# Kernel tuning notes

Measured on AMD Instinct MI355X. Metric: run time of the kernel, lower is better.

Reference implementation:

```python
import jax, jax.numpy as jnp
import numpy as np

B, S, H = 8, 512, 1024          # batch, seq_len, hidden_size
T, K, FF = 8, 2, 4096           # num_thoughts, top_k, ffn dim (4*H)
NH = 8                          # combiner attention heads
HD = H // NH
CREATIVITY = 1.0


def setup_inputs() -> dict:
    key = jax.random.key(0)
    ks = jax.random.split(key, 16)
    s = 0.02
    return {
        "hidden_states": jax.random.normal(ks[0], (B, S, H), jnp.float32),
        # router
        "router_w": jax.random.normal(ks[1], (H, T), jnp.float32) * s,
        "router_b": jnp.zeros((T,), jnp.float32),
        # thought branch FFNs (one per thought)
        "W1": jax.random.normal(ks[2], (T, H, FF), jnp.float32) * s,
        "b1": jnp.zeros((T, FF), jnp.float32),
        "W2": jax.random.normal(ks[3], (T, FF, H), jnp.float32) * s,
        "b2": jnp.zeros((T, H), jnp.float32),
        # attention combiner (MultiheadAttention proj weights)
        "Wq": jax.random.normal(ks[4], (H, H), jnp.float32) * s,
        "bq": jnp.zeros((H,), jnp.float32),
        "Wk": jax.random.normal(ks[5], (H, H), jnp.float32) * s,
        "bk": jnp.zeros((H,), jnp.float32),
        "Wv": jax.random.normal(ks[6], (H, H), jnp.float32) * s,
        "bv": jnp.zeros((H,), jnp.float32),
        "Wo": jax.random.normal(ks[7], (H, H), jnp.float32) * s,
        "bo": jnp.zeros((H,), jnp.float32),
    }


def reference(hidden_states, router_w, router_b, W1, b1, W2, b2,
              Wq, bq, Wk, bk, Wv, bv, Wo, bo):
    # ---- router: mean-pool -> linear -> softmax -> top-k ----
    pooled = hidden_states.mean(axis=1)                       # [B,H]
    router_probs = jax.nn.softmax(pooled @ router_w + router_b, axis=-1)  # [B,T]
    top_p, top_i = jax.lax.top_k(router_probs, K)             # [B,K]
    weights = jax.nn.softmax(top_p, axis=-1)                  # renormalized active weights [B,K]

    # ---- grouped branch FFN (gather expert weights, batched GEMMs) ----
    h = jnp.einsum('bsh,bkhf->bksf', hidden_states, W1[top_i]) + b1[top_i][:, :, None, :]
    h = jax.nn.gelu(h, approximate=False)
    branch_out = jnp.einsum('bksf,bkfh->bksh', h, W2[top_i]) + b2[top_i][:, :, None, :]
    branch_out = branch_out * CREATIVITY                      # [B,K,S,H]

    # ---- attention combiner over flattened thoughts [B, K*S, H] ----
    L = K * S
    flat = branch_out.reshape(B, L, H)
    q = (flat @ Wq + bq).reshape(B, L, NH, HD)
    k = (flat @ Wk + bk).reshape(B, L, NH, HD)
    v = (flat @ Wv + bv).reshape(B, L, NH, HD)
    scores = jnp.einsum('blhd,bmhd->bhlm', q, k) / jnp.sqrt(jnp.float32(HD))
    attn = jax.nn.softmax(scores, axis=-1)
    ctx = jnp.einsum('bhlm,bmhd->blhd', attn, v).reshape(B, L, H)
    attended = (ctx @ Wo + bo).reshape(B, K, S, H)

    combined = jnp.einsum('bksh,bk->bsh', attended, weights)  # [B,S,H]

    # ---- metrics ----
    entropy = jnp.mean(-jnp.sum(router_probs * jnp.log(router_probs + 1e-8), axis=1))
    a = branch_out[:, 0].reshape(B, -1)
    b_ = branch_out[:, 1].reshape(B, -1)
    cos = jnp.sum(a * b_, -1) / jnp.maximum(
        jnp.linalg.norm(a, axis=-1) * jnp.linalg.norm(b_, axis=-1), 1e-8)
    diversity = jnp.mean(1.0 - cos)
    return combined, entropy, diversity
```

## Files before the change

### kernel.cpp

```cpp
#include <hip/hip_runtime.h>
#include <hip/hip_bf16.h>
#include <math.h>

typedef float f32x4 __attribute__((ext_vector_type(4)));
typedef short s16x8 __attribute__((ext_vector_type(8)));
typedef short s16x4 __attribute__((ext_vector_type(4)));
typedef unsigned int u32;

#define DEVI __device__ __forceinline__

#define Bn   8
#define Sn   512
#define Hn   1024
#define Tn   8
#define Kn   2
#define FFn  4096
#define NHn  8
#define HDn  128
#define Ln   1024
#define OUT_COMBINED 4194304

DEVI unsigned short f2bf(float x) {
  __hip_bfloat16 h = __float2bfloat16(x);
  union { __hip_bfloat16 h; unsigned short u; } cv; cv.h = h; return cv.u;
}
DEVI float bf2f(unsigned short u) {
  union { u32 i; float f; } cv; cv.i = ((u32)u) << 16; return cv.f;
}

typedef __attribute__((address_space(3))) u32 lds_u32;
typedef __attribute__((address_space(1))) u32 glb_u32;
DEVI void gload16(const void* g, void* l) {
  __builtin_amdgcn_global_load_lds((const glb_u32*)g, (lds_u32*)l, 16, 0, 0);
}

__global__ __launch_bounds__(256) void pool_part_k(const float* __restrict__ hid, float* __restrict__ part)
{
  const int b = blockIdx.x, scn = blockIdx.y;
  const int hh = threadIdx.x * 4;
  float4 acc = make_float4(0.f, 0.f, 0.f, 0.f);
  const float* base = hid + ((long)b * Sn + (long)scn * 128) * Hn + hh;
  for (int s = 0; s < 128; ++s) {
    float4 v = *(const float4*)(base + (long)s * Hn);
    acc.x += v.x; acc.y += v.y; acc.z += v.z; acc.w += v.w;
  }
  *(float4*)(part + ((long)(scn * Bn + b)) * Hn + hh) = acc;
}

__global__ __launch_bounds__(256) void pool_final_k(const float* __restrict__ part, float* __restrict__ pooled)
{
  const int i = blockIdx.x * 256 + threadIdx.x;
  float s = 0.f;
  for (int sc = 0; sc < 4; ++sc) s += part[sc * (Bn * Hn) + i];
  pooled[i] = s * (1.f / (float)Sn);
}

__global__ __launch_bounds__(256) void router_k(
    const float* __restrict__ pooled, const float* __restrict__ rw, const float* __restrict__ rb,
    float* __restrict__ probs, int* __restrict__ topi, float* __restrict__ wts,
    int* __restrict__ flags, float* __restrict__ entropy_out)
{
  __shared__ float partial[256];
  __shared__ float lg[64];
  __shared__ int sfl[8];
  __shared__ float sent[8];
  const int tid = threadIdx.x;
  const int bt = tid & 63, slice = tid >> 6;
  const int b = bt >> 3, t = bt & 7;
  if (tid < 8) sfl[tid] = 0;
  float acc = 0.f;
  const float* pb = pooled + b * Hn;
  for (int i = slice * 256; i < slice * 256 + 256; ++i) acc += pb[i] * rw[i * Tn + t];
  partial[tid] = acc;
  __syncthreads();
  if (tid < 64) lg[tid] = rb[t] + partial[tid] + partial[tid + 64] + partial[tid + 128] + partial[tid + 192];
  __syncthreads();
  if (tid < 64 && t == 0) {
    float p[8];
    float mx = lg[b * 8];
    for (int i = 1; i < 8; ++i) mx = fmaxf(mx, lg[b * 8 + i]);
    float ssum = 0.f;
    for (int i = 0; i < 8; ++i) { p[i] = expf(lg[b * 8 + i] - mx); ssum += p[i]; }
    float ent = 0.f;
    for (int i = 0; i < 8; ++i) { p[i] /= ssum; ent -= p[i] * logf(p[i] + 1e-8f); probs[b * 8 + i] = p[i]; }
    sent[b] = ent;
    int i1 = 0;
    for (int i = 1; i < 8; ++i) if (p[i] > p[i1]) i1 = i;
    int i2 = (i1 == 0) ? 1 : 0;
    for (int i = 0; i < 8; ++i) if (i != i1 && p[i] > p[i2]) i2 = i;
    float w0 = 1.f / (1.f + expf(p[i2] - p[i1]));
    float w1 = 1.f / (1.f + expf(p[i1] - p[i2]));
    topi[b * 2] = i1; topi[b * 2 + 1] = i2;
    wts[b * 2] = w0; wts[b * 2 + 1] = w1;
    atomicOr(&sfl[i1], 1); atomicOr(&sfl[i2], 1);
  }
  __syncthreads();
  if (tid < 8) flags[tid] = sfl[tid];
  if (tid == 0) {
    float e = 0.f;
    for (int i = 0; i < 8; ++i) e += sent[i];
    entropy_out[0] = e * (1.f / (float)Bn);
  }
}

__global__ __launch_bounds__(256) void cvt_k(const float* __restrict__ in, unsigned short* __restrict__ out)
{
  const long i = ((long)blockIdx.x * 256 + threadIdx.x) * 4;
  float4 v = *(const float4*)(in + i);
  s16x4 o;
  o[0] = (short)f2bf(v.x); o[1] = (short)f2bf(v.y); o[2] = (short)f2bf(v.z); o[3] = (short)f2bf(v.w);
  *(s16x4*)(out + i) = o;
}

__global__ __launch_bounds__(256) void bias3_k(const float* __restrict__ bq, const float* __restrict__ bk,
                                               const float* __restrict__ bv, float* __restrict__ o)
{
  const int i = blockIdx.x * 256 + threadIdx.x;
  o[i] = bq[i]; o[i + 1024] = bk[i]; o[i + 2048] = bv[i];
}

__global__ __launch_bounds__(256) void transpose_k(const float* __restrict__ Win, unsigned short* __restrict__ Wout,
                                                   int Kd, int N, long sIn, long sOut, const int* __restrict__ flags)
{
  const int t = blockIdx.z;
  if (flags && flags[t] == 0) return;
  __shared__ float tile[64][65];
  const float* in = Win + (long)t * sIn;
  unsigned short* out = Wout + (long)t * sOut;
  const int kb = blockIdx.y * 64, nb = blockIdx.x * 64;
  const int tx = threadIdx.x & 15, ty = threadIdx.x >> 4;
  #pragma unroll
  for (int i = 0; i < 4; ++i) {
    const int r = ty + i * 16;
    float4 v = *(const float4*)(in + (long)(kb + r) * N + nb + tx * 4);
    tile[r][tx * 4 + 0] = v.x; tile[r][tx * 4 + 1] = v.y;
    tile[r][tx * 4 + 2] = v.z; tile[r][tx * 4 + 3] = v.w;
  }
  __syncthreads();
  #pragma unroll
  for (int i = 0; i < 4; ++i) {
    const int n = ty + i * 16;
    s16x4 o;
    #pragma unroll
    for (int j = 0; j < 4; ++j) o[j] = (short)f2bf(tile[tx * 4 + j][n]);
    *(s16x4*)(out + (long)(nb + n) * Kd + kb + tx * 4) = o;
  }
}

template<int WM, int EPI, int OUTMODE>
__global__ __launch_bounds__(WM * 256, 2) void gemm256_k(
    const unsigned short* __restrict__ A0, const unsigned short* __restrict__ Bt0,
    const float* __restrict__ bias0, unsigned short* __restrict__ C0,
    int N, int Kd,
    const int* __restrict__ topi, int kTop,
    long sA_b, long sA_p, long sBt_t, int sBias_t, long sC_p)
{
  constexpr int NBUF = (WM == 2) ? 4 : 3;
  constexpr int ASZ = WM * 8192;
  constexpr int BSZ = 16384;
  constexpr int BISS = 4 / WM;
  __shared__ __align__(16) char smem[NBUF * (ASZ + BSZ)];
  char* const Ab = smem;
  char* const Bb = smem + NBUF * ASZ;

  const int z = blockIdx.z;
  const int bidx = kTop ? (z / kTop) : 0;
  const int te = topi ? topi[z] : 0;
  const unsigned short* A = A0 + (long)bidx * sA_b + (long)z * sA_p;
  const unsigned short* Bt = Bt0 + (long)te * sBt_t;
  const float* bias = bias0 + (long)te * sBias_t;
  unsigned short* C = C0 + (long)z * sC_p;

  const int m0 = blockIdx.y * (WM * 128);
  const int n0 = blockIdx.x * 256;
  const int tid = threadIdx.x;
  const int lane = tid & 63, w = tid >> 6;
  const int wm = w >> 2, wn = w & 3;
  const int rA = lane & 15, g = lane >> 4;

  const int srow = tid >> 2;
  const int sc   = tid & 3;
  const unsigned short* gA[2];
  #pragma unroll
  for (int i = 0; i < 2; ++i) {
    const int r = i * (WM * 64) + srow;
    gA[i] = A + (long)(m0 + r) * Kd + ((sc ^ ((r >> 1) & 3)) * 8);
  }
  const unsigned short* gB[BISS];
  #pragma unroll
  for (int i = 0; i < BISS; ++i) {
    const int r = i * (WM * 64) + srow;
    gB[i] = Bt + (long)(n0 + r) * Kd + ((sc ^ ((r >> 1) & 3)) * 8);
  }
  const int sdo = tid * 16;

  int aoff[8], boff[4];
  #pragma unroll
  for (int mi = 0; mi < 8; ++mi) {
    const int row = wm * 128 + mi * 16 + rA;
    aoff[mi] = row * 64 + ((g ^ ((row >> 1) & 3)) << 4);
  }
  #pragma unroll
  for (int nj = 0; nj < 4; ++nj) {
    const int row = wn * 64 + nj * 16 + rA;
    boff[nj] = row * 64 + ((g ^ ((row >> 1) & 3)) << 4);
  }

  f32x4 acc[8][4];
  const f32x4 zero = {0.f, 0.f, 0.f, 0.f};
  #pragma unroll
  for (int i = 0; i < 8; ++i)
    #pragma unroll
    for (int j = 0; j < 4; ++j) acc[i][j] = zero;

  const int nt = Kd >> 5;

  for (int j = 0; j < NBUF - 1; ++j) {
    #pragma unroll
    for (int i = 0; i < 2; ++i)
      gload16(gA[i] + j * 32, Ab + j * ASZ + i * (WM * 4096) + sdo);
    #pragma unroll
    for (int i = 0; i < BISS; ++i)
      gload16(gB[i] + j * 32, Bb + j * BSZ + i * (WM * 4096) + sdo);
  }
  if constexpr (WM == 2) asm volatile("s_waitcnt vmcnt(8)" ::: "memory");
  else                   asm volatile("s_waitcnt vmcnt(6)" ::: "memory");
  __builtin_amdgcn_s_barrier();

  int cb = 0;
  for (int kt = 0; kt < nt; ++kt) {
    const char* pa = Ab + cb * ASZ;
    const char* pb = Bb + cb * BSZ;
    const int ft = kt + NBUF - 1;
    const int fb = (cb == 0) ? NBUF - 1 : cb - 1;
    const bool st = (ft < nt);

    s16x8 af[4], bf[4];
    #pragma unroll
    for (int mi = 0; mi < 4; ++mi) af[mi] = *(const s16x8*)(pa + aoff[mi]);
    #pragma unroll
    for (int nj = 0; nj < 4; ++nj) bf[nj] = *(const s16x8*)(pb + boff[nj]);
    if (st) {
      #pragma unroll
      for (int i = 0; i < 2; ++i)
        gload16(gA[i] + ft * 32, Ab + fb * ASZ + i * (WM * 4096) + sdo);
      if constexpr (WM == 1)
        gload16(gB[0] + ft * 32, Bb + fb * BSZ + sdo);
    }
    asm volatile("" ::: "memory");
    __builtin_amdgcn_s_barrier();
    __builtin_amdgcn_s_setprio(1);
    #pragma unroll
    for (int mi = 0; mi < 4; ++mi)
      #pragma unroll
      for (int nj = 0; nj < 4; ++nj)
        acc[mi][nj] = __builtin_amdgcn_mfma_f32_16x16x32_bf16(af[mi], bf[nj], acc[mi][nj], 0, 0, 0);
    __builtin_amdgcn_s_setprio(0);
    __builtin_amdgcn_s_barrier();

    s16x8 af2[4];
    #pragma unroll
    for (int mi = 0; mi < 4; ++mi) af2[mi] = *(const s16x8*)(pa + aoff[4 + mi]);
    if (st) {
      if constexpr (WM == 2) {
        gload16(gB[0] + ft * 32, Bb + fb * BSZ + sdo);
        gload16(gB[1] + ft * 32, Bb + fb * BSZ + 8192 + sdo);
      } else {
        gload16(gB[1] + ft * 32, Bb + fb * BSZ + 4096 + sdo);
        gload16(gB[2] + ft * 32, Bb + fb * BSZ + 8192 + sdo);
        gload16(gB[3] + ft * 32, Bb + fb * BSZ + 12288 + sdo);
      }
    }
    asm volatile("" ::: "memory");
    __builtin_amdgcn_s_barrier();
    __builtin_amdgcn_s_setprio(1);
    #pragma unroll
    for (int mi = 0; mi < 4; ++mi)
      #pragma unroll
      for (int nj = 0; nj < 4; ++nj)
        acc[4 + mi][nj] = __builtin_amdgcn_mfma_f32_16x16x32_bf16(af2[mi], bf[nj], acc[4 + mi][nj], 0, 0, 0);
    __builtin_amdgcn_s_setprio(0);

    if constexpr (WM == 2) {
      if (kt < nt - 3)       asm volatile("s_waitcnt vmcnt(8)" ::: "memory");
      else if (kt == nt - 3) asm volatile("s_waitcnt vmcnt(4)" ::: "memory");
      else if (kt == nt - 2) asm volatile("s_waitcnt vmcnt(0)" ::: "memory");
    } else {
      if (kt < nt - 2)       asm volatile("s_waitcnt vmcnt(6)" ::: "memory");
      else if (kt == nt - 2) asm volatile("s_waitcnt vmcnt(0)" ::: "memory");
    }
    __builtin_amdgcn_s_barrier();
    cb = (cb + 1 == NBUF) ? 0 : cb + 1;
  }

  __syncthreads();

  unsigned short* et = (unsigned short*)(smem + w * 9216);
  const int r4 = (lane >> 4) << 2;
  const int nbase = n0 + wn * 64;
  const int seg = (OUTMODE == 1) ? (nbase >> 10) : 0;
  const int erow = lane >> 3, echunk = lane & 7;
  float bv[4];
  #pragma unroll
  for (int nj = 0; nj < 4; ++nj) bv[nj] = bias[nbase + nj * 16 + rA];

  #pragma unroll
  for (int p = 0; p < 2; ++p) {
    #pragma unroll
    for (int nj = 0; nj < 4; ++nj) {
      #pragma unroll
      for (int mi2 = 0; mi2 < 4; ++mi2) {
        #pragma unroll
        for (int j = 0; j < 4; ++j) {
          float x = acc[p * 4 + mi2][nj][j] + bv[nj];
          if (EPI == 1) x = 0.5f * x * (1.0f + erff(x * 0.70710678118654752f));
          const int mrl = mi2 * 16 + r4 + j;
          const int ncl = nj * 16 + rA;
          if (OUTMODE == 0 || seg < 2) et[mrl * 72 + ncl] = f2bf(x);
          else                         et[ncl * 72 + mrl] = f2bf(x);
        }
      }
    }
    const long mrow0 = m0 + wm * 128 + p * 64;
    if (OUTMODE == 0) {
      #pragma unroll
      for (int rr = 0; rr < 8; ++rr) {
        const int row = rr * 8 + erow;
        s16x8 v = *(const s16x8*)(et + row * 72 + echunk * 8);
        *(s16x8*)(C + (mrow0 + row) * N + nbase + echunk * 8) = v;
      }
    } else {
      const int nseg = nbase & 1023;
      if (seg < 2) {
        unsigned short* dst = C + (long)seg * 8388608;
        #pragma unroll
        for (int rr = 0; rr < 8; ++rr) {
          const int row = rr * 8 + erow;
          s16x8 v = *(const s16x8*)(et + row * 72 + echunk * 8);
          *(s16x8*)(dst + (mrow0 + row) * 1024 + nseg + echunk * 8) = v;
        }
      } else {
        unsigned short* vtp = C + 16777216;
        const int bb = (int)(mrow0 >> 10);
        const int ltok0 = (int)(mrow0 & 1023);
        #pragma unroll
        for (int rr = 0; rr < 8; ++rr) {
          const int nrow = rr * 8 + erow;
          s16x8 v = *(const s16x8*)(et + nrow * 72 + echunk * 8);
          *(s16x8*)(vtp + ((long)(bb * 1024 + nseg + nrow)) * 1024 + ltok0 + echunk * 8) = v;
        }
      }
    }
  }
}

__global__ __launch_bounds__(256) void flash_k(
    const unsigned short* __restrict__ q, const unsigned short* __restrict__ k,
    const unsigned short* __restrict__ vt, unsigned short* __restrict__ ctx)
{
  __shared__ unsigned short Ks[64 * 128];
  __shared__ unsigned short Vs[128 * 64];
  __shared__ unsigned short Ps[4][32 * 72];
  const int qt = blockIdx.x, h = blockIdx.y, b = blockIdx.z;
  const int tid = threadIdx.x, lane = tid & 63, w = tid >> 6;
  const int rA = lane & 15, g = lane >> 4;
  const int q0w = qt * 128 + w * 32;

  s16x8 qf[2][4];
  #pragma unroll
  for (int qi = 0; qi < 2; ++qi) {
    const unsigned short* qp = q + ((long)(b * Ln + q0w + qi * 16 + rA)) * Hn + h * HDn + g * 8;
    #pragma unroll
    for (int kk = 0; kk < 4; ++kk) qf[qi][kk] = *(const s16x8*)(qp + kk * 32);
  }

  f32x4 o[2][8];
  const f32x4 zero = {0.f, 0.f, 0.f, 0.f};
  #pragma unroll
  for (int qi = 0; qi < 2; ++qi)
    #pragma unroll
    for (int nn = 0; nn < 8; ++nn) o[qi][nn] = zero;
  float lrun[2][4];
  #pragma unroll
  for (int qi = 0; qi < 2; ++qi)
    #pragma unroll
    for (int j = 0; j < 4; ++j) lrun[qi][j] = 0.f;
  float m = 0.f;

  const float sc2 = 0.08838834764831845f * 1.4426950408889634f;

  const int krow0 = w * 16 + g;
  const int kc = lane & 15;
  const int vrow0 = w * 32 + (lane >> 3);
  const int vc = lane & 7;

  for (int kvt = 0; kvt < 16; ++kvt) {
    const int kv0 = kvt * 64;
    __syncthreads();
    #pragma unroll
    for (int qq = 0; qq < 4; ++qq) {
      const int rk = krow0 + qq * 4;
      gload16(k + ((long)(b * Ln + kv0 + rk)) * Hn + h * HDn + ((kc ^ (rk & 7)) * 8),
              (char*)Ks + w * 4096 + qq * 1024);
      const int rv = vrow0 + qq * 8;
      gload16(vt + ((long)(b * 1024 + h * HDn + rv)) * Ln + kv0 + ((vc ^ (rv & 7)) * 8),
              (char*)Vs + w * 4096 + qq * 1024);
    }
    __syncthreads();

    f32x4 sacc[2][4];
    #pragma unroll
    for (int qi = 0; qi < 2; ++qi)
      #pragma unroll
      for (int nj = 0; nj < 4; ++nj) sacc[qi][nj] = zero;
    #pragma unroll
    for (int kk = 0; kk < 4; ++kk) {
      #pragma unroll
      for (int nj = 0; nj < 4; ++nj) {
        const int row = nj * 16 + rA;
        const int byt = row * 256 + (((kk * 4 + g) ^ (row & 7)) << 4);
        s16x8 kf = *(const s16x8*)((const char*)Ks + byt);
        sacc[0][nj] = __builtin_amdgcn_mfma_f32_16x16x32_bf16(qf[0][kk], kf, sacc[0][nj], 0, 0, 0);
        sacc[1][nj] = __builtin_amdgcn_mfma_f32_16x16x32_bf16(qf[1][kk], kf, sacc[1][nj], 0, 0, 0);
      }
    }

    float vmax = -3.0e38f;
    #pragma unroll
    for (int qi = 0; qi < 2; ++qi)
      #pragma unroll
      for (int nj = 0; nj < 4; ++nj)
        #pragma unroll
        for (int j = 0; j < 4; ++j) {
          const float s = sacc[qi][nj][j] * sc2;
          sacc[qi][nj][j] = s;
          vmax = fmaxf(vmax, s);
        }
    if (!__all(vmax <= m + 8.0f)) {
      float mn = vmax;
      #pragma unroll
      for (int mm = 1; mm < 64; mm <<= 1) mn = fmaxf(mn, __shfl_xor(mn, mm, 64));
      const float al = exp2f(m - mn);
      #pragma unroll
      for (int qi = 0; qi < 2; ++qi) {
        #pragma unroll
        for (int nn = 0; nn < 8; ++nn)
          #pragma unroll
          for (int j = 0; j < 4; ++j) o[qi][nn][j] *= al;
        #pragma unroll
        for (int j = 0; j < 4; ++j) lrun[qi][j] *= al;
      }
      m = mn;
    }
    #pragma unroll
    for (int qi = 0; qi < 2; ++qi)
      #pragma unroll
      for (int j = 0; j < 4; ++j) {
        float p0 = exp2f(sacc[qi][0][j] - m);
        float p1 = exp2f(sacc[qi][1][j] - m);
        float p2 = exp2f(sacc[qi][2][j] - m);
        float p3 = exp2f(sacc[qi][3][j] - m);
        lrun[qi][j] += (p0 + p1) + (p2 + p3);
        const int prow = (qi * 16 + g * 4 + j) * 72;
        Ps[w][prow + 0 * 16 + rA] = f2bf(p0);
        Ps[w][prow + 1 * 16 + rA] = f2bf(p1);
        Ps[w][prow + 2 * 16 + rA] = f2bf(p2);
        Ps[w][prow + 3 * 16 + rA] = f2bf(p3);
      }

    s16x8 pf[2][2];
    #pragma unroll
    for (int qi = 0; qi < 2; ++qi)
      #pragma unroll
      for (int kk2 = 0; kk2 < 2; ++kk2)
        pf[qi][kk2] = *(const s16x8*)(&Ps[w][(qi * 16 + rA) * 72 + kk2 * 32 + g * 8]);
    #pragma unroll
    for (int kk2 = 0; kk2 < 2; ++kk2) {
      #pragma unroll
      for (int nn = 0; nn < 8; ++nn) {
        const int row = nn * 16 + rA;
        const int byt = row * 128 + (((kk2 * 4 + g) ^ (row & 7)) << 4);
        s16x8 vf = *(const s16x8*)((const char*)Vs + byt);
        o[0][nn] = __builtin_amdgcn_mfma_f32_16x16x32_bf16(pf[0][kk2], vf, o[0][nn], 0, 0, 0);
        o[1][nn] = __builtin_amdgcn_mfma_f32_16x16x32_bf16(pf[1][kk2], vf, o[1][nn], 0, 0, 0);
      }
    }
  }

  float linv[2][4];
  #pragma unroll
  for (int qi = 0; qi < 2; ++qi)
    #pragma unroll
    for (int j = 0; j < 4; ++j) {
      float l = lrun[qi][j];
      #pragma unroll
      for (int mm = 1; mm < 16; mm <<= 1) l += __shfl_xor(l, mm, 64);
      linv[qi][j] = 1.0f / l;
    }
  #pragma unroll
  for (int qi = 0; qi < 2; ++qi)
    #pragma unroll
    for (int nn = 0; nn < 8; ++nn)
      #pragma unroll
      for (int j = 0; j < 4; ++j) {
        const int row = q0w + qi * 16 + g * 4 + j;
        ctx[((long)(b * Ln + row)) * Hn + h * HDn + nn * 16 + rA] = f2bf(o[qi][nn][j] * linv[qi][j]);
      }
}

__global__ __launch_bounds__(256) void div_part_k(const unsigned short* __restrict__ br, float* __restrict__ part)
{
  const int b = blockIdx.y, ch = blockIdx.x;
  const unsigned short* a = br + (long)b * (2L * Sn * Hn);
  const unsigned short* c = a + (long)Sn * Hn;
  const int base = ch * 16384 + threadIdx.x * 8;
  float dot = 0.f, na = 0.f, nb = 0.f;
  #pragma unroll
  for (int i = 0; i < 8; ++i) {
    const int idx = base + i * 2048;
    s16x8 av = *(const s16x8*)(a + idx);
    s16x8 cv = *(const s16x8*)(c + idx);
    #pragma unroll
    for (int e = 0; e < 8; ++e) {
      float fa = bf2f((unsigned short)av[e]);
      float fc = bf2f((unsigned short)cv[e]);
      dot += fa * fc; na += fa * fa; nb += fc * fc;
    }
  }
  #pragma unroll
  for (int mm = 1; mm < 64; mm <<= 1) {
    dot += __shfl_xor(dot, mm, 64);
    na  += __shfl_xor(na, mm, 64);
    nb  += __shfl_xor(nb, mm, 64);
  }
  __shared__ float red[12];
  const int lane = threadIdx.x & 63, w = threadIdx.x >> 6;
  if (lane == 0) { red[w * 3] = dot; red[w * 3 + 1] = na; red[w * 3 + 2] = nb; }
  __syncthreads();
  if (threadIdx.x == 0) {
    float d = 0, x = 0, y = 0;
    for (int i = 0; i < 4; ++i) { d += red[i * 3]; x += red[i * 3 + 1]; y += red[i * 3 + 2]; }
    float* op = part + ((long)(b * 32 + ch)) * 3;
    op[0] = d; op[1] = x; op[2] = y;
  }
}

__global__ __launch_bounds__(64) void div_final_k(const float* __restrict__ part, float* __restrict__ outp)
{
  __shared__ float cosr[8];
  const int tid = threadIdx.x;
  if (tid < 8) {
    float d = 0, x = 0, y = 0;
    for (int i = 0; i < 32; ++i) {
      const float* p = part + ((long)(tid * 32 + i)) * 3;
      d += p[0]; x += p[1]; y += p[2];
    }
    cosr[tid] = d / fmaxf(sqrtf(x) * sqrtf(y), 1e-8f);
  }
  __syncthreads();
  if (tid == 0) {
    float s = 0.f;
    for (int i = 0; i < 8; ++i) s += 1.f - cosr[i];
    outp[0] = s * (1.f / 8.f);
  }
}

__global__ __launch_bounds__(256) void combine_k(const unsigned short* __restrict__ att,
                                                 const float* __restrict__ wts, float* __restrict__ out)
{
  const long i = ((long)blockIdx.x * 256 + threadIdx.x) * 8;
  const int b = (int)(i >> 19);
  const long rem = i & 524287;
  const unsigned short* a0 = att + (long)b * (2L * Sn * Hn) + rem;
  const unsigned short* a1 = a0 + (long)Sn * Hn;
  const float w0 = wts[b * 2], w1 = wts[b * 2 + 1];
  s16x8 v0 = *(const s16x8*)a0;
  s16x8 v1 = *(const s16x8*)a1;
  float r[8];
  #pragma unroll
  for (int e = 0; e < 8; ++e) r[e] = w0 * bf2f((unsigned short)v0[e]) + w1 * bf2f((unsigned short)v1[e]);
  *(float4*)(out + i)     = make_float4(r[0], r[1], r[2], r[3]);
  *(float4*)(out + i + 4) = make_float4(r[4], r[5], r[6], r[7]);
}

extern "C" void kernel_launch(void* const* d_in, const int* in_sizes, int n_in,
                              void* d_out, int out_size, void* d_ws, size_t ws_size,
                              hipStream_t stream)
{
  (void)in_sizes; (void)n_in; (void)out_size; (void)ws_size;
  const float* hidden   = (const float*)d_in[0];
  const float* router_w = (const float*)d_in[1];
  const float* router_b = (const float*)d_in[2];
  const float* W1 = (const float*)d_in[3];
  const float* b1 = (const float*)d_in[4];
  const float* W2 = (const float*)d_in[5];
  const float* b2 = (const float*)d_in[6];
  const float* Wq = (const float*)d_in[7];
  const float* bq = (const float*)d_in[8];
  const float* Wk = (const float*)d_in[9];
  const float* bk = (const float*)d_in[10];
  const float* Wv = (const float*)d_in[11];
  const float* bv = (const float*)d_in[12];
  const float* Wo = (const float*)d_in[13];
  const float* bo = (const float*)d_in[14];
  float* out = (float*)d_out;

  char* ws = (char*)d_ws;
  float* pooled  = (float*)(ws);
  float* ppart   = (float*)(ws + 32768);
  float* probs   = (float*)(ws + 163840);
  int*   topi    = (int*)  (ws + 164096);
  float* wts     = (float*)(ws + 164352);
  int*   flags   = (int*)  (ws + 164608);
  float* dpart   = (float*)(ws + 164864);
  float* qkvbias = (float*)(ws + 167936);
  unsigned short* hid_bf = (unsigned short*)(ws + 262144);
  unsigned short* Wt     = (unsigned short*)(ws + 262144 + 8388608);
  unsigned short* hbuf   = (unsigned short*)(ws + 262144 + 8388608 + 67108864);
  unsigned short* br     = (unsigned short*)(ws + 262144 + 8388608 + 134217728);
  unsigned short* wqkvo  = (unsigned short*)(ws + 262144 + 8388608 + 134217728 + 16777216);
  unsigned short* qb  = Wt;
  unsigned short* kbf = Wt + 8388608;
  unsigned short* vt  = Wt + 16777216;
  unsigned short* ctx = hbuf;
  unsigned short* att = hbuf + 8388608;
  unsigned short* wqt = wqkvo;
  unsigned short* wkt = wqkvo + 1048576;
  unsigned short* wvt = wqkvo + 2097152;
  unsigned short* wot = wqkvo + 3145728;

  pool_part_k<<<dim3(Bn, 4), 256, 0, stream>>>(hidden, ppart);
  pool_final_k<<<dim3(32), 256, 0, stream>>>(ppart, pooled);
  router_k<<<1, 256, 0, stream>>>(pooled, router_w, router_b, probs, topi, wts, flags, out + OUT_COMBINED);

  cvt_k<<<4096, 256, 0, stream>>>(hidden, hid_bf);
  bias3_k<<<4, 256, 0, stream>>>(bq, bk, bv, qkvbias);
  transpose_k<<<dim3(64, 16, Tn), 256, 0, stream>>>(W1, Wt, Hn, FFn, (long)Hn * FFn, (long)FFn * Hn, flags);
  transpose_k<<<dim3(16, 16, 1), 256, 0, stream>>>(Wq, wqt, Hn, Hn, 0, 0, nullptr);
  transpose_k<<<dim3(16, 16, 1), 256, 0, stream>>>(Wk, wkt, Hn, Hn, 0, 0, nullptr);
  transpose_k<<<dim3(16, 16, 1), 256, 0, stream>>>(Wv, wvt, Hn, Hn, 0, 0, nullptr);
  transpose_k<<<dim3(16, 16, 1), 256, 0, stream>>>(Wo, wot, Hn, Hn, 0, 0, nullptr);

  gemm256_k<2, 1, 0><<<dim3(FFn / 256, Sn / 256, 16), 512, 0, stream>>>(
      hid_bf, Wt, b1, hbuf, FFn, Hn, topi, 2,
      (long)Sn * Hn, 0L, (long)FFn * Hn, FFn, (long)Sn * FFn);

  transpose_k<<<dim3(16, 64, Tn), 256, 0, stream>>>(W2, Wt, FFn, Hn, (long)FFn * Hn, (long)Hn * FFn, flags);

  gemm256_k<1, 0, 0><<<dim3(Hn / 256, Sn / 128, 16), 256, 0, stream>>>(
      hbuf, Wt, b2, br, Hn, FFn, topi, 2,
      0L, (long)Sn * FFn, (long)Hn * FFn, Hn, (long)Sn * Hn);

  div_part_k<<<dim3(32, Bn), 256, 0, stream>>>(br, dpart);
  div_final_k<<<1, 64, 0, stream>>>(dpart, out + OUT_COMBINED + 1);

  gemm256_k<2, 0, 1><<<dim3(3072 / 256, (Bn * Ln) / 256, 1), 512, 0, stream>>>(
      br, wqkvo, qkvbias, qb, 3072, Hn, nullptr, 0, 0L, 0L, 0L, 0, 0L);

  flash_k<<<dim3(Ln / 128, NHn, Bn), 256, 0, stream>>>(qb, kbf, vt, ctx);

  gemm256_k<1, 0, 0><<<dim3(Hn / 256, (Bn * Ln) / 128, 1), 256, 0, stream>>>(
      ctx, wot, bo, att, Hn, Hn, nullptr, 0, 0L, 0L, 0L, 0, 0L);

  combine_k<<<2048, 256, 0, stream>>>(att, wts, out);
}
```

Baseline: 536.6 us.

## Replace GEMM kernel with 256x128-tile variant, XCD remapping, and tanh GELU

Replaces the templated 256x256/128x256 GEMM with a single 256x128-tile, 256-thread kernel. It uses a 3-stage LDS pipeline with per-wave staging, a new swizzle, and one fewer barrier per k-step. Workgroup IDs are remapped so consecutive tiles land on the same XCD for better L2 reuse. The exact erf GELU becomes a tanh approximation via exp2, which is cheaper in the epilogue but changes numerics slightly.

```diff
diff --git a/kernel.cpp b/kernel.cpp
--- a/kernel.cpp
+++ b/kernel.cpp
@@ -26,6 +26,12 @@
 }
 DEVI float bf2f(unsigned short u) {
   union { u32 i; float f; } cv; cv.i = ((u32)u) << 16; return cv.f;
+}
+DEVI float gelu_f(float x) {
+  float t = x * x * x;
+  float y = 0.7978845608028654f * x + 0.03567740813f * t;
+  float e = exp2f(2.8853900817779268f * y);
+  return x - x / (e + 1.0f);
 }
 
 typedef __attribute__((address_space(3))) u32 lds_u32;
@@ -147,64 +153,57 @@
   }
 }
 
-template<int WM, int EPI, int OUTMODE>
-__global__ __launch_bounds__(WM * 256, 2) void gemm256_k(
+template<int EPI, int OUTMODE>
+__global__ __launch_bounds__(256, 2) void gemmT_k(
     const unsigned short* __restrict__ A0, const unsigned short* __restrict__ Bt0,
     const float* __restrict__ bias0, unsigned short* __restrict__ C0,
     int N, int Kd,
     const int* __restrict__ topi, int kTop,
     long sA_b, long sA_p, long sBt_t, int sBias_t, long sC_p)
 {
-  constexpr int NBUF = (WM == 2) ? 4 : 3;
-  constexpr int ASZ = WM * 8192;
-  constexpr int BSZ = 16384;
-  constexpr int BISS = 4 / WM;
-  __shared__ __align__(16) char smem[NBUF * (ASZ + BSZ)];
+  __shared__ __align__(16) char smem[73728];
   char* const Ab = smem;
-  char* const Bb = smem + NBUF * ASZ;
-
-  const int z = blockIdx.z;
-  const int bidx = kTop ? (z / kTop) : 0;
-  const int te = topi ? topi[z] : 0;
-  const unsigned short* A = A0 + (long)bidx * sA_b + (long)z * sA_p;
+  char* const Bb = smem + 49152;
+
+  const int gx = gridDim.x, gy = gridDim.y;
+  const int nwg = gx * gy * gridDim.z;
+  const int hw = blockIdx.x + gx * (blockIdx.y + gy * blockIdx.z);
+  const int q = nwg >> 3, r = nwg & 7;
+  const int xcd = hw & 7, sub = hw >> 3;
+  int lin = (xcd < r ? xcd * (q + 1) : r * (q + 1) + (xcd - r) * q) + sub;
+  const int bx = lin % gx; lin /= gx;
+  const int by = lin % gy;
+  const int bz = lin / gy;
+
+  const int bidx = kTop ? (bz / kTop) : 0;
+  const int te = topi ? topi[bz] : 0;
+  const unsigned short* A = A0 + (long)bidx * sA_b + (long)bz * sA_p;
   const unsigned short* Bt = Bt0 + (long)te * sBt_t;
   const float* bias = bias0 + (long)te * sBias_t;
-  unsigned short* C = C0 + (long)z * sC_p;
-
-  const int m0 = blockIdx.y * (WM * 128);
-  const int n0 = blockIdx.x * 256;
+  unsigned short* C = C0 + (long)bz * sC_p;
+
+  const int m0 = by * 256;
+  const int n0 = bx * 128;
   const int tid = threadIdx.x;
   const int lane = tid & 63, w = tid >> 6;
-  const int wm = w >> 2, wn = w & 3;
+  const int wm = w >> 1, wn = w & 1;
   const int rA = lane & 15, g = lane >> 4;
 
-  const int srow = tid >> 2;
-  const int sc   = tid & 3;
-  const unsigned short* gA[2];
-  #pragma unroll
-  for (int i = 0; i < 2; ++i) {
-    const int r = i * (WM * 64) + srow;
-    gA[i] = A + (long)(m0 + r) * Kd + ((sc ^ ((r >> 1) & 3)) * 8);
-  }
-  const unsigned short* gB[BISS];
-  #pragma unroll
-  for (int i = 0; i < BISS; ++i) {
-    const int r = i * (WM * 64) + srow;
-    gB[i] = Bt + (long)(n0 + r) * Kd + ((sc ^ ((r >> 1) & 3)) * 8);
-  }
-  const int sdo = tid * 16;
-
+  const int sr = lane >> 2;
+  const int sc = lane & 3;
+  const int csw = (sc ^ ((sr & 3) ^ ((sr >> 2) & 3))) * 8;
+  const unsigned short* gAw = A + (long)(m0 + w * 64 + sr) * Kd + csw;
+  const unsigned short* gBw = Bt + (long)(n0 + w * 32 + sr) * Kd + csw;
+  const int ldso = lane << 4;
+
+  const int sl = (rA & 3) ^ ((rA >> 2) & 3);
   int aoff[8], boff[4];
   #pragma unroll
-  for (int mi = 0; mi < 8; ++mi) {
-    const int row = wm * 128 + mi * 16 + rA;
-    aoff[mi] = row * 64 + ((g ^ ((row >> 1) & 3)) << 4);
-  }
-  #pragma unroll
-  for (int nj = 0; nj < 4; ++nj) {
-    const int row = wn * 64 + nj * 16 + rA;
-    boff[nj] = row * 64 + ((g ^ ((row >> 1) & 3)) << 4);
-  }
+  for (int mi = 0; mi < 8; ++mi)
+    aoff[mi] = (wm * 128 + mi * 16 + rA) * 64 + ((g ^ sl) << 4);
+  #pragma unroll
+  for (int nj = 0; nj < 4; ++nj)
+    boff[nj] = (wn * 64 + nj * 16 + rA) * 64 + ((g ^ sl) << 4);
 
   f32x4 acc[8][4];
   const f32x4 zero = {0.f, 0.f, 0.f, 0.f};
@@ -215,38 +214,34 @@
 
   const int nt = Kd >> 5;
 
-  for (int j = 0; j < NBUF - 1; ++j) {
-    #pragma unroll
-    for (int i = 0; i < 2; ++i)
-      gload16(gA[i] + j * 32, Ab + j * ASZ + i * (WM * 4096) + sdo);
-    #pragma unroll
-    for (int i = 0; i < BISS; ++i)
-      gload16(gB[i] + j * 32, Bb + j * BSZ + i * (WM * 4096) + sdo);
-  }
-  if constexpr (WM == 2) asm volatile("s_waitcnt vmcnt(8)" ::: "memory");
-  else                   asm volatile("s_waitcnt vmcnt(6)" ::: "memory");
+  auto stageA = [&](int kt2, int buf, int i) {
+    gload16(gAw + (long)i * 16 * Kd + kt2 * 32, Ab + buf * 16384 + w * 4096 + i * 1024 + ldso);
+  };
+  auto stageB = [&](int kt2, int buf, int i) {
+    gload16(gBw + (long)i * 16 * Kd + kt2 * 32, Bb + buf * 8192 + w * 2048 + i * 1024 + ldso);
+  };
+
+  #pragma unroll
+  for (int j = 0; j < 2; ++j) {
+    stageA(j, j, 0); stageA(j, j, 1); stageB(j, j, 0);
+    stageA(j, j, 2); stageA(j, j, 3); stageB(j, j, 1);
+  }
+  asm volatile("s_waitcnt vmcnt(6)" ::: "memory");
   __builtin_amdgcn_s_barrier();
 
-  int cb = 0;
+  int cb = 0, fb = 2;
   for (int kt = 0; kt < nt; ++kt) {
-    const char* pa = Ab + cb * ASZ;
-    const char* pb = Bb + cb * BSZ;
-    const int ft = kt + NBUF - 1;
-    const int fb = (cb == 0) ? NBUF - 1 : cb - 1;
-    const bool st = (ft < nt);
+    const char* pa = Ab + cb * 16384;
+    const char* pb = Bb + cb * 8192;
+    const bool st = (kt + 2 < nt);
+    const int ft = kt + 2;
 
     s16x8 af[4], bf[4];
     #pragma unroll
     for (int mi = 0; mi < 4; ++mi) af[mi] = *(const s16x8*)(pa + aoff[mi]);
     #pragma unroll
     for (int nj = 0; nj < 4; ++nj) bf[nj] = *(const s16x8*)(pb + boff[nj]);
-    if (st) {
-      #pragma unroll
-      for (int i = 0; i < 2; ++i)
-        gload16(gA[i] + ft * 32, Ab + fb * ASZ + i * (WM * 4096) + sdo);
-      if constexpr (WM == 1)
-        gload16(gB[0] + ft * 32, Bb + fb * BSZ + sdo);
-    }
+    if (st) { stageA(ft, fb, 0); stageA(ft, fb, 1); stageB(ft, fb, 0); }
     asm volatile("" ::: "memory");
     __builtin_amdgcn_s_barrier();
     __builtin_amdgcn_s_setprio(1);
@@ -256,21 +251,11 @@
       for (int nj = 0; nj < 4; ++nj)
         acc[mi][nj] = __builtin_amdgcn_mfma_f32_16x16x32_bf16(af[mi], bf[nj], acc[mi][nj], 0, 0, 0);
     __builtin_amdgcn_s_setprio(0);
-    __builtin_amdgcn_s_barrier();
 
     s16x8 af2[4];
     #pragma unroll
     for (int mi = 0; mi < 4; ++mi) af2[mi] = *(const s16x8*)(pa + aoff[4 + mi]);
-    if (st) {
-      if constexpr (WM == 2) {
-        gload16(gB[0] + ft * 32, Bb + fb * BSZ + sdo);
-        gload16(gB[1] + ft * 32, Bb + fb * BSZ + 8192 + sdo);
-      } else {
-        gload16(gB[1] + ft * 32, Bb + fb * BSZ + 4096 + sdo);
-        gload16(gB[2] + ft * 32, Bb + fb * BSZ + 8192 + sdo);
-        gload16(gB[3] + ft * 32, Bb + fb * BSZ + 12288 + sdo);
-      }
-    }
+    if (st) { stageA(ft, fb, 2); stageA(ft, fb, 3); stageB(ft, fb, 1); }
     asm volatile("" ::: "memory");
     __builtin_amdgcn_s_barrier();
     __builtin_amdgcn_s_setprio(1);
@@ -281,16 +266,11 @@
         acc[4 + mi][nj] = __builtin_amdgcn_mfma_f32_16x16x32_bf16(af2[mi], bf[nj], acc[4 + mi][nj], 0, 0, 0);
     __builtin_amdgcn_s_setprio(0);
 
-    if constexpr (WM == 2) {
-      if (kt < nt - 3)       asm volatile("s_waitcnt vmcnt(8)" ::: "memory");
-      else if (kt == nt - 3) asm volatile("s_waitcnt vmcnt(4)" ::: "memory");
-      else if (kt == nt - 2) asm volatile("s_waitcnt vmcnt(0)" ::: "memory");
-    } else {
-      if (kt < nt - 2)       asm volatile("s_waitcnt vmcnt(6)" ::: "memory");
-      else if (kt == nt - 2) asm volatile("s_waitcnt vmcnt(0)" ::: "memory");
-    }
+    if (st)                asm volatile("s_waitcnt vmcnt(6)" ::: "memory");
+    else if (kt + 1 < nt)  asm volatile("s_waitcnt vmcnt(0)" ::: "memory");
     __builtin_amdgcn_s_barrier();
-    cb = (cb + 1 == NBUF) ? 0 : cb + 1;
+    cb = (cb + 1 == 3) ? 0 : cb + 1;
+    fb = (fb + 1 == 3) ? 0 : fb + 1;
   }
 
   __syncthreads();
@@ -313,7 +293,7 @@
         #pragma unroll
         for (int j = 0; j < 4; ++j) {
           float x = acc[p * 4 + mi2][nj][j] + bv[nj];
-          if (EPI == 1) x = 0.5f * x * (1.0f + erff(x * 0.70710678118654752f));
+          if (EPI == 1) x = gelu_f(x);
           const int mrl = mi2 * 16 + r4 + j;
           const int ncl = nj * 16 + rA;
           if (OUTMODE == 0 || seg < 2) et[mrl * 72 + ncl] = f2bf(x);
@@ -641,25 +621,25 @@
   transpose_k<<<dim3(16, 16, 1), 256, 0, stream>>>(Wv, wvt, Hn, Hn, 0, 0, nullptr);
   transpose_k<<<dim3(16, 16, 1), 256, 0, stream>>>(Wo, wot, Hn, Hn, 0, 0, nullptr);
 
-  gemm256_k<2, 1, 0><<<dim3(FFn / 256, Sn / 256, 16), 512, 0, stream>>>(
+  gemmT_k<1, 0><<<dim3(FFn / 128, Sn / 256, 16), 256, 0, stream>>>(
       hid_bf, Wt, b1, hbuf, FFn, Hn, topi, 2,
       (long)Sn * Hn, 0L, (long)FFn * Hn, FFn, (long)Sn * FFn);
 
   transpose_k<<<dim3(16, 64, Tn), 256, 0, stream>>>(W2, Wt, FFn, Hn, (long)FFn * Hn, (long)Hn * FFn, flags);
 
-  gemm256_k<1, 0, 0><<<dim3(Hn / 256, Sn / 128, 16), 256, 0, stream>>>(
+  gemmT_k<0, 0><<<dim3(Hn / 128, Sn / 256, 16), 256, 0, stream>>>(
       hbuf, Wt, b2, br, Hn, FFn, topi, 2,
       0L, (long)Sn * FFn, (long)Hn * FFn, Hn, (long)Sn * Hn);
 
   div_part_k<<<dim3(32, Bn), 256, 0, stream>>>(br, dpart);
   div_final_k<<<1, 64, 0, stream>>>(dpart, out + OUT_COMBINED + 1);
 
-  gemm256_k<2, 0, 1><<<dim3(3072 / 256, (Bn * Ln) / 256, 1), 512, 0, stream>>>(
+  gemmT_k<0, 1><<<dim3(3072 / 128, (Bn * Ln) / 256, 1), 256, 0, stream>>>(
       br, wqkvo, qkvbias, qb, 3072, Hn, nullptr, 0, 0L, 0L, 0L, 0, 0L);
 
   flash_k<<<dim3(Ln / 128, NHn, Bn), 256, 0, stream>>>(qb, kbf, vt, ctx);
 
-  gemm256_k<1, 0, 0><<<dim3(Hn / 256, (Bn * Ln) / 128, 1), 256, 0, stream>>>(
+  gemmT_k<0, 0><<<dim3(Hn / 128, (Bn * Ln) / 256, 1), 256, 0, stream>>>(
       ctx, wot, bo, att, Hn, Hn, nullptr, 0, 0L, 0L, 0L, 0, 0L);
 
   combine_k<<<2048, 256, 0, stream>>>(att, wts, out);
```

After: 523.9 us. 2.4% less time.
